# Kernel tuning notes

Measured on AMD Instinct MI355X. Metric: run time of the kernel, lower is better.

Reference implementation:

```python
import jax, jax.numpy as jnp
import numpy as np

N, E = 50000, 800000
IN, HID, HEADS, OUT, EDIM = 128, 32, 4, 40, 5
HC = HEADS * HID  # 128, conv1 output width


def setup_inputs() -> dict:
    key = jax.random.key(0)
    ks = jax.random.split(key, 24)
    p = lambda i, shape: (jax.random.normal(ks[i], shape, jnp.float32) * 0.1)
    return {
        "x": jax.random.normal(ks[0], (N, IN), jnp.float32),
        "edge_index": jax.random.randint(ks[1], (2, E), 0, N, jnp.int32),
        "edge_attr": jax.random.normal(ks[2], (E, EDIM), jnp.float32),
        # GATConv layer 1 (in -> hidden, heads=4)
        "W1": p(3, (IN, HC)), "att_src1": p(4, (HEADS, HID)), "att_dst1": p(5, (HEADS, HID)),
        "att_edge1": p(6, (HEADS, HID)), "We1": p(7, (EDIM, HC)), "b1": p(8, (HC,)),
        # GATConv layer 2 (hidden*heads -> out, heads=1)
        "W2": p(9, (HC, OUT)), "att_src2": p(10, (1, OUT)), "att_dst2": p(11, (1, OUT)),
        "att_edge2": p(12, (1, OUT)), "We2": p(13, (EDIM, OUT)), "b2": p(14, (OUT,)),
        # BatchNorm (eval mode: running stats)
        "g1": jnp.ones((HC,), jnp.float32), "be1": p(15, (HC,)),
        "rm1": p(16, (HC,)), "rv1": jnp.ones((HC,), jnp.float32),
        "g2": jnp.ones((OUT,), jnp.float32), "be2": p(17, (OUT,)),
        "rm2": p(18, (OUT,)), "rv2": jnp.ones((OUT,), jnp.float32),
    }


def gat_conv(x, src, dst, eattr, W, a_src, a_dst, a_edge, We, b, H, C):
    n = x.shape[0]
    xs = (x @ W).reshape(n, H, C)                       # shared lin for src/dst (PyG)
    alpha_s = jnp.einsum('nhc,hc->nh', xs, a_src)       # [N,H]
    alpha_d = jnp.einsum('nhc,hc->nh', xs, a_dst)       # [N,H]
    e = (eattr @ We).reshape(-1, H, C)                  # [E',H,C]
    alpha_e = jnp.einsum('ehc,hc->eh', e, a_edge)       # [E',H]
    alpha = jax.nn.leaky_relu(alpha_s[src] + alpha_d[dst] + alpha_e, 0.2)
    # segment softmax over incoming edges of each dst node
    amax = jax.ops.segment_max(alpha, dst, num_segments=n)
    ex = jnp.exp(alpha - amax[dst])
    denom = jax.ops.segment_sum(ex, dst, num_segments=n)
    coef = ex / (denom[dst] + 1e-16)                    # [E',H]
    out = jax.ops.segment_sum(xs[src] * coef[:, :, None], dst, num_segments=n)
    return out.reshape(n, H * C) + b                    # concat heads + bias


def batch_norm_eval(x, g, be, rm, rv):
    return g * (x - rm) * jax.lax.rsqrt(rv + 1e-5) + be


def reference(x, edge_index, edge_attr, W1, att_src1, att_dst1, att_edge1, We1, b1,
              W2, att_src2, att_dst2, att_edge2, We2, b2,
              g1, be1, rm1, rv1, g2, be2, rm2, rv2):
    src0, dst0 = edge_index[0], edge_index[1]
    # add self loops with fill_value='mean': loop edge_attr = mean of incoming edge_attr
    cnt = jax.ops.segment_sum(jnp.ones((E,), x.dtype), dst0, num_segments=N)
    loop_attr = jax.ops.segment_sum(edge_attr, dst0, num_segments=N) / jnp.maximum(cnt, 1.0)[:, None]
    loop = jnp.arange(N, dtype=src0.dtype)
    src = jnp.concatenate([src0, loop])
    dst = jnp.concatenate([dst0, loop])
    ea = jnp.concatenate([edge_attr, loop_attr], axis=0)
    # layer 1 (dropout = identity in eval)
    h = gat_conv(x, src, dst, ea, W1, att_src1, att_dst1, att_edge1, We1, b1, HEADS, HID)
    h = jax.nn.elu(batch_norm_eval(h, g1, be1, rm1, rv1))
    # layer 2 (heads=1)
    h = gat_conv(h, src, dst, ea, W2, att_src2, att_dst2, att_edge2, We2, b2, 1, OUT)
    h = batch_norm_eval(h, g2, be2, rm2, rv2)
    return jax.nn.log_softmax(h, axis=1)
```

## Files before the change

kernel.cpp:

```cpp
#include <hip/hip_runtime.h>
#include <hip/hip_bf16.h>

#define NN 50000
#define NE 800000
#define SCAN_NB ((NN + 255) / 256)

typedef float f32x4_t __attribute__((ext_vector_type(4)));
typedef float f32x2_t __attribute__((ext_vector_type(2)));
typedef short s16x8_t __attribute__((ext_vector_type(8)));

__device__ __forceinline__ unsigned f2bf2(float a, float b) {
    unsigned ua = __float_as_uint(a);
    ua = (ua + 0x7fffu + ((ua >> 16) & 1u)) >> 16;
    unsigned ub = __float_as_uint(b);
    ub = (ub + 0x7fffu + ((ub >> 16) & 1u)) >> 16;
    return ua | (ub << 16);
}
__device__ __forceinline__ float bf_lo(unsigned u) { return __uint_as_float(u << 16); }
__device__ __forceinline__ float bf_hi(unsigned u) { return __uint_as_float(u & 0xffff0000u); }
__device__ __forceinline__ f32x2_t bfpair(unsigned u) {
    return (f32x2_t){__uint_as_float(u << 16), __uint_as_float(u & 0xffff0000u)};
}

__global__ __launch_bounds__(256) void prep_kernel(
    const float* __restrict__ We1, const float* __restrict__ ae1w,
    const float* __restrict__ We2, const float* __restrict__ ae2w,
    const float* __restrict__ W1, const float* __restrict__ W2,
    float* __restrict__ wf1, float* __restrict__ wf2,
    unsigned* __restrict__ w1t, unsigned* __restrict__ w2t,
    int* __restrict__ cnt) {
    int t = threadIdx.x;
    int g = blockIdx.x * 256 + t;
    if (g < NN) cnt[g] = 0;
    if (blockIdx.x != 0) return;
    if (t < 20) {
        int j = t >> 2, h = t & 3;
        float s = 0.f;
        for (int c = 0; c < 32; ++c) s += We1[j * 128 + h * 32 + c] * ae1w[h * 32 + c];
        wf1[j * 4 + h] = s;
    }
    if (t >= 32 && t < 37) {
        int j = t - 32;
        float s = 0.f;
        for (int c = 0; c < 40; ++c) s += We2[j * 40 + c] * ae2w[c];
        wf2[j] = s;
    }
    for (int i = t; i < 128 * 64; i += 256) {
        int c = i >> 6, kp = i & 63;
        w1t[i] = f2bf2(W1[(size_t)(2 * kp) * 128 + c], W1[(size_t)(2 * kp + 1) * 128 + c]);
    }
    for (int i = t; i < 48 * 64; i += 256) {
        int c = i >> 6, kp = i & 63;
        w2t[i] = (c < 40) ? f2bf2(W2[(size_t)(2 * kp) * 40 + c], W2[(size_t)(2 * kp + 1) * 40 + c]) : 0u;
    }
}

__global__ __launch_bounds__(256) void count_kernel(const int* __restrict__ dst0,
                                                    int* __restrict__ cnt,
                                                    int* __restrict__ rank) {
    int e = blockIdx.x * 256 + threadIdx.x;
    if (e >= NE) return;
    rank[e] = atomicAdd(&cnt[dst0[e]], 1);
}

__global__ __launch_bounds__(256) void scan1_kernel(const int* __restrict__ cnt,
                                                    int* __restrict__ off,
                                                    int* __restrict__ bsum) {
    __shared__ int tmp[256];
    int t = threadIdx.x;
    int g = blockIdx.x * 256 + t;
    int v = (g < NN) ? cnt[g] : 0;
    tmp[t] = v;
    __syncthreads();
#pragma unroll
    for (int d = 1; d < 256; d <<= 1) {
        int u = (t >= d) ? tmp[t - d] : 0;
        __syncthreads();
        tmp[t] += u;
        __syncthreads();
    }
    if (g < NN) off[g] = tmp[t] - v;
    if (t == 255) bsum[blockIdx.x] = tmp[255];
}

__global__ __launch_bounds__(256) void scan2_kernel(int* __restrict__ bsum) {
    __shared__ int tmp[256];
    int t = threadIdx.x;
    int v = (t < SCAN_NB) ? bsum[t] : 0;
    tmp[t] = v;
    __syncthreads();
#pragma unroll
    for (int d = 1; d < 256; d <<= 1) {
        int u = (t >= d) ? tmp[t - d] : 0;
        __syncthreads();
        tmp[t] += u;
        __syncthreads();
    }
    if (t < SCAN_NB) bsum[t] = tmp[t] - v;
}

__global__ __launch_bounds__(256) void scan3_kernel(int* __restrict__ off,
                                                    const int* __restrict__ bsum,
                                                    const int* __restrict__ cnt) {
    int g = blockIdx.x * 256 + threadIdx.x;
    if (g < NN) {
        int o = off[g] + bsum[blockIdx.x];
        off[g] = o;
        if (g == NN - 1) off[NN] = o + cnt[g];
    }
}

__global__ __launch_bounds__(256) void fill_fold_kernel(
    const int* __restrict__ src0, const int* __restrict__ dst0,
    const float* __restrict__ eattr, const float* __restrict__ wf1,
    const float* __restrict__ wf2, const int* __restrict__ off,
    const int* __restrict__ rank, uint4* __restrict__ epk) {
    int base = blockIdx.x * 1024 + threadIdx.x;
#pragma unroll
    for (int k = 0; k < 4; ++k) {
        int e = base + k * 256;
        if (e >= NE) continue;
        float a[5];
#pragma unroll
        for (int j = 0; j < 5; ++j) a[j] = eattr[(size_t)e * 5 + j];
        float o[4];
#pragma unroll
        for (int h = 0; h < 4; ++h) {
            float s = 0.f;
#pragma unroll
            for (int j = 0; j < 5; ++j) s += a[j] * wf1[j * 4 + h];
            o[h] = s;
        }
        float s2 = 0.f;
#pragma unroll
        for (int j = 0; j < 5; ++j) s2 += a[j] * wf2[j];
        int pos = off[dst0[e]] + rank[e];
        epk[pos] = make_uint4((unsigned)src0[e], f2bf2(o[0], o[1]), f2bf2(o[2], o[3]),
                              __float_as_uint(s2));
    }
}

__global__ __launch_bounds__(256) void gemm1_mfma(
    const float* __restrict__ A, const unsigned* __restrict__ w1t,
    unsigned* __restrict__ out) {
    __shared__ unsigned sA[64 * 68];
    __shared__ unsigned sB[128 * 68];
    int t = threadIdx.x;
    int row0 = blockIdx.x * 64;
    for (int i = t; i < 64 * 32; i += 256) {
        int r = i >> 5, q = i & 31;
        int gr = row0 + r;
        float4 v = (gr < NN) ? *(const float4*)&A[(size_t)gr * 128 + q * 4]
                             : make_float4(0.f, 0.f, 0.f, 0.f);
        sA[r * 68 + q * 2]     = f2bf2(v.x, v.y);
        sA[r * 68 + q * 2 + 1] = f2bf2(v.z, v.w);
    }
    for (int i = t; i < 128 * 16; i += 256) {
        int c = i >> 4, q = i & 15;
        *(uint4*)&sB[c * 68 + q * 4] = *(const uint4*)&w1t[c * 64 + q * 4];
    }
    __syncthreads();
    int wv = t >> 6, lane = t & 63;
    int lr = lane & 15, kgrp = lane >> 4;
    f32x4_t acc[8];
#pragma unroll
    for (int i = 0; i < 8; ++i) acc[i] = (f32x4_t){0.f, 0.f, 0.f, 0.f};
    int arow = wv * 16 + lr;
#pragma unroll
    for (int kt = 0; kt < 4; ++kt) {
        int kw = kt * 16 + kgrp * 4;
        s16x8_t af = *(const s16x8_t*)&sA[arow * 68 + kw];
#pragma unroll
        for (int tc = 0; tc < 8; ++tc) {
            s16x8_t bf = *(const s16x8_t*)&sB[(tc * 16 + lr) * 68 + kw];
            acc[tc] = __builtin_amdgcn_mfma_f32_16x16x32_bf16(af, bf, acc[tc], 0, 0, 0);
        }
    }
    int orow0 = row0 + wv * 16 + kgrp * 4;
#pragma unroll
    for (int tc = 0; tc < 8; ++tc) {
#pragma unroll
        for (int r = 0; r < 4; ++r) {
            float v = acc[tc][r];
            float other = __shfl_xor(v, 1);
            int gr = orow0 + r;
            if (!(lane & 1) && gr < NN)
                out[(size_t)gr * 64 + tc * 8 + (lr >> 1)] = f2bf2(v, other);
        }
    }
}

__global__ __launch_bounds__(256) void alpha1_kernel(
    const unsigned* __restrict__ xs1u, const float* __restrict__ asw,
    const float* __restrict__ adw, float* __restrict__ as1, float* __restrict__ ad1) {
    int wid = (blockIdx.x * 256 + threadIdx.x) >> 6;
    if (wid >= NN) return;
    int lane = threadIdx.x & 63;
    int c = lane * 2;
    unsigned u = xs1u[(size_t)wid * 64 + lane];
    float vx = bf_lo(u), vy = bf_hi(u);
    float pa = vx * asw[c] + vy * asw[c + 1];
    float pd = vx * adw[c] + vy * adw[c + 1];
#pragma unroll
    for (int d = 8; d >= 1; d >>= 1) {
        pa += __shfl_xor(pa, d, 16);
        pd += __shfl_xor(pd, d, 16);
    }
    if ((lane & 15) == 0) {
        as1[wid * 4 + (lane >> 4)] = pa;
        ad1[wid * 4 + (lane >> 4)] = pd;
    }
}

__global__ __launch_bounds__(256) void gat1_kernel(
    const uint4* __restrict__ epk, const int* __restrict__ off,
    const unsigned* __restrict__ xs1u,
    const float4* __restrict__ as1, const float4* __restrict__ ad1,
    const float* __restrict__ b1, const float* __restrict__ g1, const float* __restrict__ be1,
    const float* __restrict__ rm1, const float* __restrict__ rv1, unsigned* __restrict__ h1u) {
    __shared__ int   lds_s[4][4][16];
    __shared__ float lds_w[4][4][16][4];
    int wave = threadIdx.x >> 6;
    int lane = threadIdx.x & 63;
    int g = lane >> 4;
    int lr = lane & 15;
    int qh = lr >> 2;
    int n = blockIdx.x * 16 + wave * 4 + g;
    int e0 = off[n];
    int deg = off[n + 1] - e0;
    float4 adn = ad1[n];
    float4 asn = as1[n];
    f32x2_t acc2[4];
#pragma unroll
    for (int k = 0; k < 4; ++k) acc2[k] = (f32x2_t){0.f, 0.f};
    float ds0 = 0.f, ds1 = 0.f, ds2 = 0.f, ds3 = 0.f;
    float s0 = 0.f, s1 = 0.f, s2 = 0.f, s3 = 0.f;
    int mc = (deg + 15) >> 4;
    mc = max(mc, __shfl_xor(mc, 16));
    mc = max(mc, __shfl_xor(mc, 32));

    for (int ch = 0; ch < mc; ++ch) {
        int i = ch * 16 + lr;
        int s = 0;
        float w0 = 0.f, w1 = 0.f, w2 = 0.f, w3 = 0.f;
        if (i < deg) {
            uint4 ep = epk[e0 + i];
            s = (int)ep.x;
            float ax = bf_lo(ep.y), ay = bf_hi(ep.y);
            float az = bf_lo(ep.z), aw = bf_hi(ep.z);
            float4 av = as1[s];
            float a0 = av.x + adn.x + ax;
            float a1 = av.y + adn.y + ay;
            float a2 = av.z + adn.z + az;
            float a3 = av.w + adn.w + aw;
            a0 = a0 >= 0.f ? a0 : 0.2f * a0;
            a1 = a1 >= 0.f ? a1 : 0.2f * a1;
            a2 = a2 >= 0.f ? a2 : 0.2f * a2;
            a3 = a3 >= 0.f ? a3 : 0.2f * a3;
            w0 = __expf(a0); w1 = __expf(a1); w2 = __expf(a2); w3 = __expf(a3);
            ds0 += w0; ds1 += w1; ds2 += w2; ds3 += w3;
            s0 += ax; s1 += ay; s2 += az; s3 += aw;
        }
        lds_s[wave][g][lr] = s;
        *(float4*)&lds_w[wave][g][lr][0] = make_float4(w0, w1, w2, w3);
        __builtin_amdgcn_wave_barrier();
        int cn = deg - ch * 16;
        cn = cn > 16 ? 16 : (cn < 0 ? 0 : cn);
        int cnr = (cn + 3) & ~3;
        for (int j = 0; j < cnr; j += 4) {
            int sj0 = lds_s[wave][g][j];
            int sj1 = lds_s[wave][g][j + 1];
            int sj2 = lds_s[wave][g][j + 2];
            int sj3 = lds_s[wave][g][j + 3];
            float ww0 = lds_w[wave][g][j][qh];
            float ww1 = lds_w[wave][g][j + 1][qh];
            float ww2 = lds_w[wave][g][j + 2][qh];
            float ww3 = lds_w[wave][g][j + 3][qh];
            uint4 u0 = *(const uint4*)&xs1u[(size_t)sj0 * 64 + lr * 4];
            uint4 u1 = *(const uint4*)&xs1u[(size_t)sj1 * 64 + lr * 4];
            uint4 u2 = *(const uint4*)&xs1u[(size_t)sj2 * 64 + lr * 4];
            uint4 u3 = *(const uint4*)&xs1u[(size_t)sj3 * 64 + lr * 4];
            f32x2_t W0 = {ww0, ww0}, W1v = {ww1, ww1}, W2v = {ww2, ww2}, W3v = {ww3, ww3};
            acc2[0] += W0 * bfpair(u0.x); acc2[1] += W0 * bfpair(u0.y);
            acc2[2] += W0 * bfpair(u0.z); acc2[3] += W0 * bfpair(u0.w);
            acc2[0] += W1v * bfpair(u1.x); acc2[1] += W1v * bfpair(u1.y);
            acc2[2] += W1v * bfpair(u1.z); acc2[3] += W1v * bfpair(u1.w);
            acc2[0] += W2v * bfpair(u2.x); acc2[1] += W2v * bfpair(u2.y);
            acc2[2] += W2v * bfpair(u2.z); acc2[3] += W2v * bfpair(u2.w);
            acc2[0] += W3v * bfpair(u3.x); acc2[1] += W3v * bfpair(u3.y);
            acc2[2] += W3v * bfpair(u3.z); acc2[3] += W3v * bfpair(u3.w);
        }
        __builtin_amdgcn_wave_barrier();
    }
#pragma unroll
    for (int d = 8; d >= 1; d >>= 1) {
        ds0 += __shfl_xor(ds0, d, 16); ds1 += __shfl_xor(ds1, d, 16);
        ds2 += __shfl_xor(ds2, d, 16); ds3 += __shfl_xor(ds3, d, 16);
        s0 += __shfl_xor(s0, d, 16);   s1 += __shfl_xor(s1, d, 16);
        s2 += __shfl_xor(s2, d, 16);   s3 += __shfl_xor(s3, d, 16);
    }
    float invd = 1.f / fmaxf((float)deg, 1.f);
    float aL0 = asn.x + adn.x + s0 * invd;
    float aL1 = asn.y + adn.y + s1 * invd;
    float aL2 = asn.z + adn.z + s2 * invd;
    float aL3 = asn.w + adn.w + s3 * invd;
    aL0 = aL0 >= 0.f ? aL0 : 0.2f * aL0;
    aL1 = aL1 >= 0.f ? aL1 : 0.2f * aL1;
    aL2 = aL2 >= 0.f ? aL2 : 0.2f * aL2;
    aL3 = aL3 >= 0.f ? aL3 : 0.2f * aL3;
    float ws0 = __expf(aL0), ws1 = __expf(aL1), ws2 = __expf(aL2), ws3 = __expf(aL3);
    float wself = qh == 0 ? ws0 : (qh == 1 ? ws1 : (qh == 2 ? ws2 : ws3));
    float dh = qh == 0 ? ds0 + ws0 : (qh == 1 ? ds1 + ws1 : (qh == 2 ? ds2 + ws2 : ds3 + ws3));
    uint4 us = *(const uint4*)&xs1u[(size_t)n * 64 + lr * 4];
    f32x2_t Ws = {wself, wself};
    acc2[0] += Ws * bfpair(us.x); acc2[1] += Ws * bfpair(us.y);
    acc2[2] += Ws * bfpair(us.z); acc2[3] += Ws * bfpair(us.w);
    float inv = 1.f / (dh + 1e-16f);
    int c = lr * 8;
    uint4 ou;
    unsigned* op = (unsigned*)&ou;
#pragma unroll
    for (int k2 = 0; k2 < 4; ++k2) {
        int c0 = c + 2 * k2, c1 = c + 2 * k2 + 1;
        float o0 = acc2[k2][0] * inv + b1[c0];
        float o1 = acc2[k2][1] * inv + b1[c1];
        float sc0 = g1[c0] * rsqrtf(rv1[c0] + 1e-5f);
        float sc1 = g1[c1] * rsqrtf(rv1[c1] + 1e-5f);
        o0 = (o0 - rm1[c0]) * sc0 + be1[c0];
        o1 = (o1 - rm1[c1]) * sc1 + be1[c1];
        o0 = o0 > 0.f ? o0 : __expf(o0) - 1.f;
        o1 = o1 > 0.f ? o1 : __expf(o1) - 1.f;
        op[k2] = f2bf2(o0, o1);
    }
    *(uint4*)&h1u[(size_t)n * 64 + lr * 4] = ou;
}

__global__ __launch_bounds__(256) void gemm2_mfma(
    const unsigned* __restrict__ A, const unsigned* __restrict__ w2t,
    unsigned* __restrict__ out) {
    __shared__ unsigned sA[64 * 68];
    __shared__ unsigned sB[48 * 68];
    int t = threadIdx.x;
    int row0 = blockIdx.x * 64;
    for (int i = t; i < 64 * 16; i += 256) {
        int r = i >> 4, q = i & 15;
        int gr = row0 + r;
        uint4 v = (gr < NN) ? *(const uint4*)&A[(size_t)gr * 64 + q * 4]
                            : make_uint4(0u, 0u, 0u, 0u);
        *(uint4*)&sA[r * 68 + q * 4] = v;
    }
    for (int i = t; i < 48 * 16; i += 256) {
        int c = i >> 4, q = i & 15;
        *(uint4*)&sB[c * 68 + q * 4] = *(const uint4*)&w2t[c * 64 + q * 4];
    }
    __syncthreads();
    int wv = t >> 6, lane = t & 63;
    int lr = lane & 15, kgrp = lane >> 4;
    f32x4_t acc[3];
#pragma unroll
    for (int i = 0; i < 3; ++i) acc[i] = (f32x4_t){0.f, 0.f, 0.f, 0.f};
    int arow = wv * 16 + lr;
#pragma unroll
    for (int kt = 0; kt < 4; ++kt) {
        int kw = kt * 16 + kgrp * 4;
        s16x8_t af = *(const s16x8_t*)&sA[arow * 68 + kw];
#pragma unroll
        for (int tc = 0; tc < 3; ++tc) {
            s16x8_t bf = *(const s16x8_t*)&sB[(tc * 16 + lr) * 68 + kw];
            acc[tc] = __builtin_amdgcn_mfma_f32_16x16x32_bf16(af, bf, acc[tc], 0, 0, 0);
        }
    }
    int orow0 = row0 + wv * 16 + kgrp * 4;
#pragma unroll
    for (int tc = 0; tc < 3; ++tc) {
#pragma unroll
        for (int r = 0; r < 4; ++r) {
            float v = acc[tc][r];
            float other = __shfl_xor(v, 1);
            int gr = orow0 + r;
            if (!(lane & 1) && gr < NN && (tc < 2 || lr < 8))
                out[(size_t)gr * 32 + tc * 8 + (lr >> 1)] = f2bf2(v, other);
        }
    }
}

__global__ __launch_bounds__(256) void alpha2_kernel(
    const unsigned* __restrict__ xs2u, const float* __restrict__ asw,
    const float* __restrict__ adw, float* __restrict__ as2, float* __restrict__ ad2) {
    int wid = (blockIdx.x * 256 + threadIdx.x) >> 6;
    if (wid >= NN) return;
    int lane = threadIdx.x & 63;
    float pa = 0.f, pd = 0.f;
    if (lane < 20) {
        unsigned u = xs2u[(size_t)wid * 32 + lane];
        float vx = bf_lo(u), vy = bf_hi(u);
        int c = lane * 2;
        pa = vx * asw[c] + vy * asw[c + 1];
        pd = vx * adw[c] + vy * adw[c + 1];
    }
#pragma unroll
    for (int d = 16; d >= 1; d >>= 1) {
        pa += __shfl_xor(pa, d, 32);
        pd += __shfl_xor(pd, d, 32);
    }
    if (lane == 0) { as2[wid] = pa; ad2[wid] = pd; }
}

__global__ __launch_bounds__(256) void gat2_kernel(
    const uint4* __restrict__ epk, const int* __restrict__ off,
    const unsigned* __restrict__ xs2u,
    const float* __restrict__ as2, const float* __restrict__ ad2,
    const float* __restrict__ b2, const float* __restrict__ g2, const float* __restrict__ be2,
    const float* __restrict__ rm2, const float* __restrict__ rv2, float* __restrict__ outp) {
    __shared__ int   lds_s[4][72];
    __shared__ float lds_w[4][72];
    int wid = (blockIdx.x * 256 + threadIdx.x) >> 6;
    if (wid >= NN) return;
    int lane = threadIdx.x & 63;
    int warp = threadIdx.x >> 6;
    int n = wid;
    int e0 = off[n], e1 = off[n + 1];
    int deg = e1 - e0;
    int grp3 = lane / 20;
    int col = lane - grp3 * 20;
    bool act = grp3 < 3;
    int grpo = act ? grp3 : 0;
    if (lane < 8) {
        lds_s[warp][64 + lane] = 0;
        lds_w[warp][64 + lane] = 0.f;
    }
    float adn = ad2[n];
    float asn = as2[n];
    f32x2_t acc2 = {0.f, 0.f};
    float dsum = 0.f, aesum = 0.f;

    for (int base = 0; base < deg; base += 64) {
        int i = base + lane;
        int cn = min(64, deg - base);
        int s = 0;
        float w = 0.f;
        if (i < deg) {
            uint4 ep = epk[e0 + i];
            s = (int)ep.x;
            float ae = __uint_as_float(ep.w);
            float a = as2[s] + adn + ae;
            a = a >= 0.f ? a : 0.2f * a;
            w = __expf(a);
            dsum += w;
            aesum += ae;
        }
        lds_s[warp][lane] = s;
        lds_w[warp][lane] = w;
        __builtin_amdgcn_wave_barrier();
        int cnr = ((cn + 11) / 12) * 12;
        for (int j = 0; j < cnr; j += 12) {
            int jj0 = j + grpo, jj1 = jj0 + 3, jj2 = jj0 + 6, jj3 = jj0 + 9;
            int sj0 = lds_s[warp][jj0];
            int sj1 = lds_s[warp][jj1];
            int sj2 = lds_s[warp][jj2];
            int sj3 = lds_s[warp][jj3];
            float w0 = act ? lds_w[warp][jj0] : 0.f;
            float w1 = act ? lds_w[warp][jj1] : 0.f;
            float w2 = act ? lds_w[warp][jj2] : 0.f;
            float w3 = act ? lds_w[warp][jj3] : 0.f;
            unsigned u0 = xs2u[(size_t)sj0 * 32 + col];
            unsigned u1 = xs2u[(size_t)sj1 * 32 + col];
            unsigned u2 = xs2u[(size_t)sj2 * 32 + col];
            unsigned u3 = xs2u[(size_t)sj3 * 32 + col];
            acc2 += (f32x2_t){w0, w0} * bfpair(u0);
            acc2 += (f32x2_t){w1, w1} * bfpair(u1);
            acc2 += (f32x2_t){w2, w2} * bfpair(u2);
            acc2 += (f32x2_t){w3, w3} * bfpair(u3);
        }
        __builtin_amdgcn_wave_barrier();
    }
    {
        float p0 = __shfl(acc2[0], (lane + 20) & 63);
        float p1 = __shfl(acc2[1], (lane + 20) & 63);
        float q0 = __shfl(acc2[0], (lane + 40) & 63);
        float q1 = __shfl(acc2[1], (lane + 40) & 63);
        acc2[0] += p0 + q0;
        acc2[1] += p1 + q1;
    }
#pragma unroll
    for (int d = 32; d >= 1; d >>= 1) {
        dsum += __shfl_xor(dsum, d);
        aesum += __shfl_xor(aesum, d);
    }
    float invd = 1.f / fmaxf((float)deg, 1.f);
    float aL = asn + adn + aesum * invd;
    aL = aL >= 0.f ? aL : 0.2f * aL;
    float wself = __expf(aL);
    float denom = dsum + wself;

    float v0 = 0.f, v1 = 0.f;
    if (lane < 20) {
        unsigned u = xs2u[(size_t)n * 32 + lane];
        acc2[0] += wself * bf_lo(u);
        acc2[1] += wself * bf_hi(u);
        int c = lane * 2;
        float inv = 1.f / (denom + 1e-16f);
        v0 = acc2[0] * inv + b2[c];
        v1 = acc2[1] * inv + b2[c + 1];
        float sc0 = g2[c] * rsqrtf(rv2[c] + 1e-5f);
        float sc1 = g2[c + 1] * rsqrtf(rv2[c + 1] + 1e-5f);
        v0 = (v0 - rm2[c]) * sc0 + be2[c];
        v1 = (v1 - rm2[c + 1]) * sc1 + be2[c + 1];
    }
    float mx = (lane < 20) ? fmaxf(v0, v1) : -3.0e38f;
#pragma unroll
    for (int d = 32; d >= 1; d >>= 1) mx = fmaxf(mx, __shfl_xor(mx, d));
    float ex = (lane < 20) ? __expf(v0 - mx) + __expf(v1 - mx) : 0.f;
#pragma unroll
    for (int d = 32; d >= 1; d >>= 1) ex += __shfl_xor(ex, d);
    if (lane < 20) {
        float ls = __logf(ex);
        *(float2*)&outp[(size_t)n * 40 + lane * 2] = make_float2(v0 - mx - ls, v1 - mx - ls);
    }
}

extern "C" void kernel_launch(void* const* d_in, const int* in_sizes, int n_in,
                              void* d_out, int out_size, void* d_ws, size_t ws_size,
                              hipStream_t stream) {
    const float* x     = (const float*)d_in[0];
    const int*   ei    = (const int*)d_in[1];
    const float* eattr = (const float*)d_in[2];
    const float* W1    = (const float*)d_in[3];
    const float* as1w  = (const float*)d_in[4];
    const float* ad1w  = (const float*)d_in[5];
    const float* ae1w  = (const float*)d_in[6];
    const float* We1   = (const float*)d_in[7];
    const float* b1    = (const float*)d_in[8];
    const float* W2    = (const float*)d_in[9];
    const float* as2w  = (const float*)d_in[10];
    const float* ad2w  = (const float*)d_in[11];
    const float* ae2w  = (const float*)d_in[12];
    const float* We2   = (const float*)d_in[13];
    const float* b2    = (const float*)d_in[14];
    const float* g1    = (const float*)d_in[15];
    const float* be1   = (const float*)d_in[16];
    const float* rm1   = (const float*)d_in[17];
    const float* rv1   = (const float*)d_in[18];
    const float* g2    = (const float*)d_in[19];
    const float* be2   = (const float*)d_in[20];
    const float* rm2   = (const float*)d_in[21];
    const float* rv2   = (const float*)d_in[22];

    const int* src0 = ei;
    const int* dst0 = ei + NE;

    char* p = (char*)d_ws;
    auto take = [&](size_t nbytes) {
        void* r = (void*)p;
        p += (nbytes + 255) & ~(size_t)255;
        return r;
    };
    float*    wf1    = (float*)take(80);
    float*    wf2    = (float*)take(20);
    unsigned* w1t    = (unsigned*)take((size_t)128 * 64 * 4);
    unsigned* w2t    = (unsigned*)take((size_t)48 * 64 * 4);
    int*      cnt    = (int*)take((size_t)NN * 4);
    int*      off    = (int*)take((size_t)(NN + 1) * 4);
    int*      bsum   = (int*)take((size_t)SCAN_NB * 4);
    int*      rank   = (int*)take((size_t)NE * 4);
    uint4*    epk    = (uint4*)take((size_t)NE * 16);
    float*    as1    = (float*)take((size_t)NN * 16);
    float*    ad1    = (float*)take((size_t)NN * 16);
    float*    as2    = (float*)take((size_t)NN * 4);
    float*    ad2    = (float*)take((size_t)NN * 4);
    unsigned* xs1u   = (unsigned*)take((size_t)NN * 256);
    unsigned* h1u    = (unsigned*)take((size_t)NN * 256);
    unsigned* xs2u   = (unsigned*)take((size_t)NN * 128);

    prep_kernel<<<SCAN_NB, 256, 0, stream>>>(We1, ae1w, We2, ae2w, W1, W2, wf1, wf2,
                                             w1t, w2t, cnt);
    count_kernel<<<(NE + 255) / 256, 256, 0, stream>>>(dst0, cnt, rank);
    scan1_kernel<<<SCAN_NB, 256, 0, stream>>>(cnt, off, bsum);
    scan2_kernel<<<1, 256, 0, stream>>>(bsum);
    scan3_kernel<<<SCAN_NB, 256, 0, stream>>>(off, bsum, cnt);
    fill_fold_kernel<<<(NE + 1023) / 1024, 256, 0, stream>>>(src0, dst0, eattr, wf1, wf2,
                                                             off, rank, epk);
    gemm1_mfma<<<(NN + 63) / 64, 256, 0, stream>>>(x, w1t, xs1u);
    alpha1_kernel<<<(NN + 3) / 4, 256, 0, stream>>>(xs1u, as1w, ad1w, as1, ad1);
    gat1_kernel<<<NN / 16, 256, 0, stream>>>(epk, off, xs1u, (const float4*)as1,
                                             (const float4*)ad1, b1, g1, be1, rm1, rv1, h1u);
    gemm2_mfma<<<(NN + 63) / 64, 256, 0, stream>>>(h1u, w2t, xs2u);
    alpha2_kernel<<<(NN + 3) / 4, 256, 0, stream>>>(xs2u, as2w, ad2w, as2, ad2);
    gat2_kernel<<<(NN + 3) / 4, 256, 0, stream>>>(epk, off, xs2u, as2, ad2,
                                                  b2, g2, be2, rm2, rv2, (float*)d_out);
}
```

Measured before the change: 180.1 us.

## Fuse independent launches and merge gat1, gemm2, alpha2 into one kernel

Result: no change. 182.4 us (+1.3%).

```diff
diff --git a/kernel.cpp b/kernel.cpp
--- a/kernel.cpp
+++ b/kernel.cpp
@@ -4,6 +4,9 @@
 #define NN 50000
 #define NE 800000
 #define SCAN_NB ((NN + 255) / 256)
+#define CNT_NB ((NE + 255) / 256)
+#define G1_NB ((NN + 63) / 64)
+#define A1_NB ((NN + 3) / 4)
 
 typedef float f32x4_t __attribute__((ext_vector_type(4)));
 typedef float f32x2_t __attribute__((ext_vector_type(2)));
@@ -55,32 +58,101 @@
     }
 }
 
-__global__ __launch_bounds__(256) void count_kernel(const int* __restrict__ dst0,
-                                                    int* __restrict__ cnt,
-                                                    int* __restrict__ rank) {
-    int e = blockIdx.x * 256 + threadIdx.x;
-    if (e >= NE) return;
-    rank[e] = atomicAdd(&cnt[dst0[e]], 1);
-}
-
-__global__ __launch_bounds__(256) void scan1_kernel(const int* __restrict__ cnt,
-                                                    int* __restrict__ off,
-                                                    int* __restrict__ bsum) {
-    __shared__ int tmp[256];
+__global__ __launch_bounds__(256) void count_gemm1(
+    const int* __restrict__ dst0, int* __restrict__ cnt, int* __restrict__ rank,
+    const float* __restrict__ A, const unsigned* __restrict__ w1t,
+    unsigned* __restrict__ out) {
+    if (blockIdx.x < CNT_NB) {
+        int e = blockIdx.x * 256 + threadIdx.x;
+        if (e < NE) rank[e] = atomicAdd(&cnt[dst0[e]], 1);
+        return;
+    }
+    __shared__ unsigned sA[64 * 68];
+    __shared__ unsigned sB[128 * 68];
     int t = threadIdx.x;
-    int g = blockIdx.x * 256 + t;
-    int v = (g < NN) ? cnt[g] : 0;
-    tmp[t] = v;
+    int row0 = (blockIdx.x - CNT_NB) * 64;
+    for (int i = t; i < 64 * 32; i += 256) {
+        int r = i >> 5, q = i & 31;
+        int gr = row0 + r;
+        float4 v = (gr < NN) ? *(const float4*)&A[(size_t)gr * 128 + q * 4]
+                             : make_float4(0.f, 0.f, 0.f, 0.f);
+        sA[r * 68 + q * 2]     = f2bf2(v.x, v.y);
+        sA[r * 68 + q * 2 + 1] = f2bf2(v.z, v.w);
+    }
+    for (int i = t; i < 128 * 16; i += 256) {
+        int c = i >> 4, q = i & 15;
+        *(uint4*)&sB[c * 68 + q * 4] = *(const uint4*)&w1t[c * 64 + q * 4];
+    }
     __syncthreads();
-#pragma unroll
-    for (int d = 1; d < 256; d <<= 1) {
-        int u = (t >= d) ? tmp[t - d] : 0;
+    int wv = t >> 6, lane = t & 63;
+    int lr = lane & 15, kgrp = lane >> 4;
+    f32x4_t acc[8];
+#pragma unroll
+    for (int i = 0; i < 8; ++i) acc[i] = (f32x4_t){0.f, 0.f, 0.f, 0.f};
+    int arow = wv * 16 + lr;
+#pragma unroll
+    for (int kt = 0; kt < 4; ++kt) {
+        int kw = kt * 16 + kgrp * 4;
+        s16x8_t af = *(const s16x8_t*)&sA[arow * 68 + kw];
+#pragma unroll
+        for (int tc = 0; tc < 8; ++tc) {
+            s16x8_t bf = *(const s16x8_t*)&sB[(tc * 16 + lr) * 68 + kw];
+            acc[tc] = __builtin_amdgcn_mfma_f32_16x16x32_bf16(af, bf, acc[tc], 0, 0, 0);
+        }
+    }
+    int orow0 = row0 + wv * 16 + kgrp * 4;
+#pragma unroll
+    for (int tc = 0; tc < 8; ++tc) {
+#pragma unroll
+        for (int r = 0; r < 4; ++r) {
+            float v = acc[tc][r];
+            float other = __shfl_xor(v, 1);
+            int gr = orow0 + r;
+            if (!(lane & 1) && gr < NN)
+                out[(size_t)gr * 64 + tc * 8 + (lr >> 1)] = f2bf2(v, other);
+        }
+    }
+}
+
+__global__ __launch_bounds__(256) void scan1_alpha1(
+    const int* __restrict__ cnt, int* __restrict__ off, int* __restrict__ bsum,
+    const unsigned* __restrict__ xs1u, const float* __restrict__ asw,
+    const float* __restrict__ adw, float* __restrict__ as1, float* __restrict__ ad1) {
+    if (blockIdx.x < SCAN_NB) {
+        __shared__ int tmp[256];
+        int t = threadIdx.x;
+        int g = blockIdx.x * 256 + t;
+        int v = (g < NN) ? cnt[g] : 0;
+        tmp[t] = v;
         __syncthreads();
-        tmp[t] += u;
-        __syncthreads();
-    }
-    if (g < NN) off[g] = tmp[t] - v;
-    if (t == 255) bsum[blockIdx.x] = tmp[255];
+#pragma unroll
+        for (int d = 1; d < 256; d <<= 1) {
+            int u = (t >= d) ? tmp[t - d] : 0;
+            __syncthreads();
+            tmp[t] += u;
+            __syncthreads();
+        }
+        if (g < NN) off[g] = tmp[t] - v;
+        if (t == 255) bsum[blockIdx.x] = tmp[255];
+        return;
+    }
+    int wid = ((blockIdx.x - SCAN_NB) * 256 + threadIdx.x) >> 6;
+    if (wid >= NN) return;
+    int lane = threadIdx.x & 63;
+    int c = lane * 2;
+    unsigned u = xs1u[(size_t)wid * 64 + lane];
+    float vx = bf_lo(u), vy = bf_hi(u);
+    float pa = vx * asw[c] + vy * asw[c + 1];
+    float pd = vx * adw[c] + vy * adw[c + 1];
+#pragma unroll
+    for (int d = 8; d >= 1; d >>= 1) {
+        pa += __shfl_xor(pa, d, 16);
+        pd += __shfl_xor(pd, d, 16);
+    }
+    if ((lane & 15) == 0) {
+        as1[wid * 4 + (lane >> 4)] = pa;
+        ad1[wid * 4 + (lane >> 4)] = pd;
+    }
 }
 
 __global__ __launch_bounds__(256) void scan2_kernel(int* __restrict__ bsum) {
@@ -140,96 +212,45 @@
     }
 }
 
-__global__ __launch_bounds__(256) void gemm1_mfma(
-    const float* __restrict__ A, const unsigned* __restrict__ w1t,
-    unsigned* __restrict__ out) {
-    __shared__ unsigned sA[64 * 68];
-    __shared__ unsigned sB[128 * 68];
-    int t = threadIdx.x;
-    int row0 = blockIdx.x * 64;
-    for (int i = t; i < 64 * 32; i += 256) {
-        int r = i >> 5, q = i & 31;
-        int gr = row0 + r;
-        float4 v = (gr < NN) ? *(const float4*)&A[(size_t)gr * 128 + q * 4]
-                             : make_float4(0.f, 0.f, 0.f, 0.f);
-        sA[r * 68 + q * 2]     = f2bf2(v.x, v.y);
-        sA[r * 68 + q * 2 + 1] = f2bf2(v.z, v.w);
-    }
-    for (int i = t; i < 128 * 16; i += 256) {
-        int c = i >> 4, q = i & 15;
-        *(uint4*)&sB[c * 68 + q * 4] = *(const uint4*)&w1t[c * 64 + q * 4];
-    }
-    __syncthreads();
-    int wv = t >> 6, lane = t & 63;
-    int lr = lane & 15, kgrp = lane >> 4;
-    f32x4_t acc[8];
-#pragma unroll
-    for (int i = 0; i < 8; ++i) acc[i] = (f32x4_t){0.f, 0.f, 0.f, 0.f};
-    int arow = wv * 16 + lr;
-#pragma unroll
-    for (int kt = 0; kt < 4; ++kt) {
-        int kw = kt * 16 + kgrp * 4;
-        s16x8_t af = *(const s16x8_t*)&sA[arow * 68 + kw];
-#pragma unroll
-        for (int tc = 0; tc < 8; ++tc) {
-            s16x8_t bf = *(const s16x8_t*)&sB[(tc * 16 + lr) * 68 + kw];
-            acc[tc] = __builtin_amdgcn_mfma_f32_16x16x32_bf16(af, bf, acc[tc], 0, 0, 0);
-        }
-    }
-    int orow0 = row0 + wv * 16 + kgrp * 4;
-#pragma unroll
-    for (int tc = 0; tc < 8; ++tc) {
-#pragma unroll
-        for (int r = 0; r < 4; ++r) {
-            float v = acc[tc][r];
-            float other = __shfl_xor(v, 1);
-            int gr = orow0 + r;
-            if (!(lane & 1) && gr < NN)
-                out[(size_t)gr * 64 + tc * 8 + (lr >> 1)] = f2bf2(v, other);
-        }
-    }
-}
-
-__global__ __launch_bounds__(256) void alpha1_kernel(
-    const unsigned* __restrict__ xs1u, const float* __restrict__ asw,
-    const float* __restrict__ adw, float* __restrict__ as1, float* __restrict__ ad1) {
-    int wid = (blockIdx.x * 256 + threadIdx.x) >> 6;
-    if (wid >= NN) return;
-    int lane = threadIdx.x & 63;
-    int c = lane * 2;
-    unsigned u = xs1u[(size_t)wid * 64 + lane];
-    float vx = bf_lo(u), vy = bf_hi(u);
-    float pa = vx * asw[c] + vy * asw[c + 1];
-    float pd = vx * adw[c] + vy * adw[c + 1];
-#pragma unroll
-    for (int d = 8; d >= 1; d >>= 1) {
-        pa += __shfl_xor(pa, d, 16);
-        pd += __shfl_xor(pd, d, 16);
-    }
-    if ((lane & 15) == 0) {
-        as1[wid * 4 + (lane >> 4)] = pa;
-        ad1[wid * 4 + (lane >> 4)] = pd;
-    }
-}
-
-__global__ __launch_bounds__(256) void gat1_kernel(
+__global__ __launch_bounds__(1024) void layer2_fused(
     const uint4* __restrict__ epk, const int* __restrict__ off,
     const unsigned* __restrict__ xs1u,
     const float4* __restrict__ as1, const float4* __restrict__ ad1,
     const float* __restrict__ b1, const float* __restrict__ g1, const float* __restrict__ be1,
-    const float* __restrict__ rm1, const float* __restrict__ rv1, unsigned* __restrict__ h1u) {
-    __shared__ int   lds_s[4][4][16];
-    __shared__ float lds_w[4][4][16][4];
-    int wave = threadIdx.x >> 6;
-    int lane = threadIdx.x & 63;
+    const float* __restrict__ rm1, const float* __restrict__ rv1,
+    const unsigned* __restrict__ w2t, const float* __restrict__ as2w,
+    const float* __restrict__ ad2w, unsigned* __restrict__ xs2u,
+    float* __restrict__ as2, float* __restrict__ ad2) {
+    __shared__ unsigned hA[64 * 68];
+    __shared__ unsigned sB[48 * 68];
+    __shared__ int   lds_s[16][4][16];
+    __shared__ float lds_w[16][4][16][4];
+    __shared__ unsigned hX[64 * 24];
+
+    int tid = threadIdx.x;
+    int wave = tid >> 6;
+    int lane = tid & 63;
     int g = lane >> 4;
     int lr = lane & 15;
     int qh = lr >> 2;
-    int n = blockIdx.x * 16 + wave * 4 + g;
-    int e0 = off[n];
-    int deg = off[n + 1] - e0;
-    float4 adn = ad1[n];
-    float4 asn = as1[n];
+    int row0 = blockIdx.x * 64;
+    int rhat = wave * 4 + g;
+    int n = row0 + rhat;
+    bool valid = n < NN;
+
+    if (tid < 48 * 16) {
+        int c = tid >> 4, q = tid & 15;
+        *(uint4*)&sB[c * 68 + q * 4] = *(const uint4*)&w2t[c * 64 + q * 4];
+    }
+
+    int e0 = 0, deg = 0;
+    float4 adn = make_float4(0.f, 0.f, 0.f, 0.f), asn = adn;
+    if (valid) {
+        e0 = off[n];
+        deg = off[n + 1] - e0;
+        adn = ad1[n];
+        asn = as1[n];
+    }
     f32x2_t acc2[4];
 #pragma unroll
     for (int k = 0; k < 4; ++k) acc2[k] = (f32x2_t){0.f, 0.f};
@@ -299,111 +320,90 @@
         s0 += __shfl_xor(s0, d, 16);   s1 += __shfl_xor(s1, d, 16);
         s2 += __shfl_xor(s2, d, 16);   s3 += __shfl_xor(s3, d, 16);
     }
-    float invd = 1.f / fmaxf((float)deg, 1.f);
-    float aL0 = asn.x + adn.x + s0 * invd;
-    float aL1 = asn.y + adn.y + s1 * invd;
-    float aL2 = asn.z + adn.z + s2 * invd;
-    float aL3 = asn.w + adn.w + s3 * invd;
-    aL0 = aL0 >= 0.f ? aL0 : 0.2f * aL0;
-    aL1 = aL1 >= 0.f ? aL1 : 0.2f * aL1;
-    aL2 = aL2 >= 0.f ? aL2 : 0.2f * aL2;
-    aL3 = aL3 >= 0.f ? aL3 : 0.2f * aL3;
-    float ws0 = __expf(aL0), ws1 = __expf(aL1), ws2 = __expf(aL2), ws3 = __expf(aL3);
-    float wself = qh == 0 ? ws0 : (qh == 1 ? ws1 : (qh == 2 ? ws2 : ws3));
-    float dh = qh == 0 ? ds0 + ws0 : (qh == 1 ? ds1 + ws1 : (qh == 2 ? ds2 + ws2 : ds3 + ws3));
-    uint4 us = *(const uint4*)&xs1u[(size_t)n * 64 + lr * 4];
-    f32x2_t Ws = {wself, wself};
-    acc2[0] += Ws * bfpair(us.x); acc2[1] += Ws * bfpair(us.y);
-    acc2[2] += Ws * bfpair(us.z); acc2[3] += Ws * bfpair(us.w);
-    float inv = 1.f / (dh + 1e-16f);
-    int c = lr * 8;
-    uint4 ou;
-    unsigned* op = (unsigned*)&ou;
-#pragma unroll
-    for (int k2 = 0; k2 < 4; ++k2) {
-        int c0 = c + 2 * k2, c1 = c + 2 * k2 + 1;
-        float o0 = acc2[k2][0] * inv + b1[c0];
-        float o1 = acc2[k2][1] * inv + b1[c1];
-        float sc0 = g1[c0] * rsqrtf(rv1[c0] + 1e-5f);
-        float sc1 = g1[c1] * rsqrtf(rv1[c1] + 1e-5f);
-        o0 = (o0 - rm1[c0]) * sc0 + be1[c0];
-        o1 = (o1 - rm1[c1]) * sc1 + be1[c1];
-        o0 = o0 > 0.f ? o0 : __expf(o0) - 1.f;
-        o1 = o1 > 0.f ? o1 : __expf(o1) - 1.f;
-        op[k2] = f2bf2(o0, o1);
-    }
-    *(uint4*)&h1u[(size_t)n * 64 + lr * 4] = ou;
-}
-
-__global__ __launch_bounds__(256) void gemm2_mfma(
-    const unsigned* __restrict__ A, const unsigned* __restrict__ w2t,
-    unsigned* __restrict__ out) {
-    __shared__ unsigned sA[64 * 68];
-    __shared__ unsigned sB[48 * 68];
-    int t = threadIdx.x;
-    int row0 = blockIdx.x * 64;
-    for (int i = t; i < 64 * 16; i += 256) {
-        int r = i >> 4, q = i & 15;
-        int gr = row0 + r;
-        uint4 v = (gr < NN) ? *(const uint4*)&A[(size_t)gr * 64 + q * 4]
-                            : make_uint4(0u, 0u, 0u, 0u);
-        *(uint4*)&sA[r * 68 + q * 4] = v;
-    }
-    for (int i = t; i < 48 * 16; i += 256) {
-        int c = i >> 4, q = i & 15;
-        *(uint4*)&sB[c * 68 + q * 4] = *(const uint4*)&w2t[c * 64 + q * 4];
-    }
+    uint4 ou = make_uint4(0u, 0u, 0u, 0u);
+    if (valid) {
+        float invd = 1.f / fmaxf((float)deg, 1.f);
+        float aL0 = asn.x + adn.x + s0 * invd;
+        float aL1 = asn.y + adn.y + s1 * invd;
+        float aL2 = asn.z + adn.z + s2 * invd;
+        float aL3 = asn.w + adn.w + s3 * invd;
+        aL0 = aL0 >= 0.f ? aL0 : 0.2f * aL0;
+        aL1 = aL1 >= 0.f ? aL1 : 0.2f * aL1;
+        aL2 = aL2 >= 0.f ? aL2 : 0.2f * aL2;
+        aL3 = aL3 >= 0.f ? aL3 : 0.2f * aL3;
+        float ws0 = __expf(aL0), ws1 = __expf(aL1), ws2 = __expf(aL2), ws3 = __expf(aL3);
+        float wself = qh == 0 ? ws0 : (qh == 1 ? ws1 : (qh == 2 ? ws2 : ws3));
+        float dh = qh == 0 ? ds0 + ws0 : (qh == 1 ? ds1 + ws1 : (qh == 2 ? ds2 + ws2 : ds3 + ws3));
+        uint4 us = *(const uint4*)&xs1u[(size_t)n * 64 + lr * 4];
+        f32x2_t Ws = {wself, wself};
+        acc2[0] += Ws * bfpair(us.x); acc2[1] += Ws * bfpair(us.y);
+        acc2[2] += Ws * bfpair(us.z); acc2[3] += Ws * bfpair(us.w);
+        float inv = 1.f / (dh + 1e-16f);
+        int c = lr * 8;
+        unsigned* op = (unsigned*)&ou;
+#pragma unroll
+        for (int k2 = 0; k2 < 4; ++k2) {
+            int c0 = c + 2 * k2, c1 = c + 2 * k2 + 1;
+            float o0 = acc2[k2][0] * inv + b1[c0];
+            float o1 = acc2[k2][1] * inv + b1[c1];
+            float sc0 = g1[c0] * rsqrtf(rv1[c0] + 1e-5f);
+            float sc1 = g1[c1] * rsqrtf(rv1[c1] + 1e-5f);
+            o0 = (o0 - rm1[c0]) * sc0 + be1[c0];
+            o1 = (o1 - rm1[c1]) * sc1 + be1[c1];
+            o0 = o0 > 0.f ? o0 : __expf(o0) - 1.f;
+            o1 = o1 > 0.f ? o1 : __expf(o1) - 1.f;
+            op[k2] = f2bf2(o0, o1);
+        }
+    }
+    *(uint4*)&hA[rhat * 68 + lr * 4] = ou;
     __syncthreads();
-    int wv = t >> 6, lane = t & 63;
-    int lr = lane & 15, kgrp = lane >> 4;
-    f32x4_t acc[3];
-#pragma unroll
-    for (int i = 0; i < 3; ++i) acc[i] = (f32x4_t){0.f, 0.f, 0.f, 0.f};
-    int arow = wv * 16 + lr;
-#pragma unroll
-    for (int kt = 0; kt < 4; ++kt) {
-        int kw = kt * 16 + kgrp * 4;
-        s16x8_t af = *(const s16x8_t*)&sA[arow * 68 + kw];
-#pragma unroll
-        for (int tc = 0; tc < 3; ++tc) {
+
+    if (wave < 12) {
+        int rowgrp = wave & 3, tc = wave >> 2;
+        int kgrp = lane >> 4;
+        int arow = rowgrp * 16 + lr;
+        f32x4_t acc = (f32x4_t){0.f, 0.f, 0.f, 0.f};
+#pragma unroll
+        for (int kt = 0; kt < 4; ++kt) {
+            int kw = kt * 16 + kgrp * 4;
+            s16x8_t af = *(const s16x8_t*)&hA[arow * 68 + kw];
             s16x8_t bf = *(const s16x8_t*)&sB[(tc * 16 + lr) * 68 + kw];
-            acc[tc] = __builtin_amdgcn_mfma_f32_16x16x32_bf16(af, bf, acc[tc], 0, 0, 0);
-        }
-    }
-    int orow0 = row0 + wv * 16 + kgrp * 4;
-#pragma unroll
-    for (int tc = 0; tc < 3; ++tc) {
+            acc = __builtin_amdgcn_mfma_f32_16x16x32_bf16(af, bf, acc, 0, 0, 0);
+        }
+        int orow = rowgrp * 16 + kgrp * 4;
 #pragma unroll
         for (int r = 0; r < 4; ++r) {
-            float v = acc[tc][r];
+            float v = acc[r];
             float other = __shfl_xor(v, 1);
-            int gr = orow0 + r;
-            if (!(lane & 1) && gr < NN && (tc < 2 || lr < 8))
-                out[(size_t)gr * 32 + tc * 8 + (lr >> 1)] = f2bf2(v, other);
-        }
-    }
-}
-
-__global__ __launch_bounds__(256) void alpha2_kernel(
-    const unsigned* __restrict__ xs2u, const float* __restrict__ asw,
-    const float* __restrict__ adw, float* __restrict__ as2, float* __restrict__ ad2) {
-    int wid = (blockIdx.x * 256 + threadIdx.x) >> 6;
-    if (wid >= NN) return;
-    int lane = threadIdx.x & 63;
-    float pa = 0.f, pd = 0.f;
-    if (lane < 20) {
-        unsigned u = xs2u[(size_t)wid * 32 + lane];
-        float vx = bf_lo(u), vy = bf_hi(u);
-        int c = lane * 2;
-        pa = vx * asw[c] + vy * asw[c + 1];
-        pd = vx * adw[c] + vy * adw[c + 1];
-    }
-#pragma unroll
-    for (int d = 16; d >= 1; d >>= 1) {
-        pa += __shfl_xor(pa, d, 32);
-        pd += __shfl_xor(pd, d, 32);
-    }
-    if (lane == 0) { as2[wid] = pa; ad2[wid] = pd; }
+            int gr = row0 + orow + r;
+            if (!(lane & 1) && gr < NN && (tc < 2 || lr < 8)) {
+                unsigned u = f2bf2(v, other);
+                xs2u[(size_t)gr * 32 + tc * 8 + (lr >> 1)] = u;
+                hX[(orow + r) * 24 + tc * 8 + (lr >> 1)] = u;
+            }
+        }
+    }
+    __syncthreads();
+
+#pragma unroll
+    for (int k = 0; k < 4; ++k) {
+        int rr = wave * 4 + k;
+        int gr = row0 + rr;
+        float pa = 0.f, pd = 0.f;
+        if (lane < 20) {
+            unsigned u = hX[rr * 24 + lane];
+            float vx = bf_lo(u), vy = bf_hi(u);
+            int c = lane * 2;
+            pa = vx * as2w[c] + vy * as2w[c + 1];
+            pd = vx * ad2w[c] + vy * ad2w[c + 1];
+        }
+#pragma unroll
+        for (int d = 16; d >= 1; d >>= 1) {
+            pa += __shfl_xor(pa, d, 32);
+            pd += __shfl_xor(pd, d, 32);
+        }
+        if (lane == 0 && gr < NN) { as2[gr] = pa; ad2[gr] = pd; }
+    }
 }
 
 __global__ __launch_bounds__(256) void gat2_kernel(
@@ -569,23 +569,20 @@
     float*    as2    = (float*)take((size_t)NN * 4);
     float*    ad2    = (float*)take((size_t)NN * 4);
     unsigned* xs1u   = (unsigned*)take((size_t)NN * 256);
-    unsigned* h1u    = (unsigned*)take((size_t)NN * 256);
     unsigned* xs2u   = (unsigned*)take((size_t)NN * 128);
 
     prep_kernel<<<SCAN_NB, 256, 0, stream>>>(We1, ae1w, We2, ae2w, W1, W2, wf1, wf2,
                                              w1t, w2t, cnt);
-    count_kernel<<<(NE + 255) / 256, 256, 0, stream>>>(dst0, cnt, rank);
-    scan1_kernel<<<SCAN_NB, 256, 0, stream>>>(cnt, off, bsum);
+    count_gemm1<<<CNT_NB + G1_NB, 256, 0, stream>>>(dst0, cnt, rank, x, w1t, xs1u);
+    scan1_alpha1<<<SCAN_NB + A1_NB, 256, 0, stream>>>(cnt, off, bsum, xs1u, as1w, ad1w,
+                                                      as1, ad1);
     scan2_kernel<<<1, 256, 0, stream>>>(bsum);
     scan3_kernel<<<SCAN_NB, 256, 0, stream>>>(off, bsum, cnt);
     fill_fold_kernel<<<(NE + 1023) / 1024, 256, 0, stream>>>(src0, dst0, eattr, wf1, wf2,
                                                              off, rank, epk);
-    gemm1_mfma<<<(NN + 63) / 64, 256, 0, stream>>>(x, w1t, xs1u);
-    alpha1_kernel<<<(NN + 3) / 4, 256, 0, stream>>>(xs1u, as1w, ad1w, as1, ad1);
-    gat1_kernel<<<NN / 16, 256, 0, stream>>>(epk, off, xs1u, (const float4*)as1,
-                                             (const float4*)ad1, b1, g1, be1, rm1, rv1, h1u);
-    gemm2_mfma<<<(NN + 63) / 64, 256, 0, stream>>>(h1u, w2t, xs2u);
-    alpha2_kernel<<<(NN + 3) / 4, 256, 0, stream>>>(xs2u, as2w, ad2w, as2, ad2);
+    layer2_fused<<<G1_NB, 1024, 0, stream>>>(epk, off, xs1u, (const float4*)as1,
+                                             (const float4*)ad1, b1, g1, be1, rm1, rv1,
+                                             w2t, as2w, ad2w, xs2u, as2, ad2);
     gat2_kernel<<<(NN + 3) / 4, 256, 0, stream>>>(epk, off, xs2u, as2, ad2,
                                                   b2, g2, be2, rm2, rv2, (float*)d_out);
 }
```

## Merge independent CSR build and GEMM1 stages into fewer horizontally fused launches

Applied to the files above, without the earlier changes.

After: 172.7 us. 1.04x faster.

```diff
diff --git a/kernel.cpp b/kernel.cpp
--- a/kernel.cpp
+++ b/kernel.cpp
@@ -4,6 +4,9 @@
 #define NN 50000
 #define NE 800000
 #define SCAN_NB ((NN + 255) / 256)
+#define CNT_NB ((NE + 255) / 256)
+#define G1_NB ((NN + 63) / 64)
+#define A1_NB ((NN + 3) / 4)
 
 typedef float f32x4_t __attribute__((ext_vector_type(4)));
 typedef float f32x2_t __attribute__((ext_vector_type(2)));
@@ -55,98 +58,19 @@
     }
 }
 
-__global__ __launch_bounds__(256) void count_kernel(const int* __restrict__ dst0,
-                                                    int* __restrict__ cnt,
-                                                    int* __restrict__ rank) {
-    int e = blockIdx.x * 256 + threadIdx.x;
-    if (e >= NE) return;
-    rank[e] = atomicAdd(&cnt[dst0[e]], 1);
-}
-
-__global__ __launch_bounds__(256) void scan1_kernel(const int* __restrict__ cnt,
-                                                    int* __restrict__ off,
-                                                    int* __restrict__ bsum) {
-    __shared__ int tmp[256];
-    int t = threadIdx.x;
-    int g = blockIdx.x * 256 + t;
-    int v = (g < NN) ? cnt[g] : 0;
-    tmp[t] = v;
-    __syncthreads();
-#pragma unroll
-    for (int d = 1; d < 256; d <<= 1) {
-        int u = (t >= d) ? tmp[t - d] : 0;
-        __syncthreads();
-        tmp[t] += u;
-        __syncthreads();
-    }
-    if (g < NN) off[g] = tmp[t] - v;
-    if (t == 255) bsum[blockIdx.x] = tmp[255];
-}
-
-__global__ __launch_bounds__(256) void scan2_kernel(int* __restrict__ bsum) {
-    __shared__ int tmp[256];
-    int t = threadIdx.x;
-    int v = (t < SCAN_NB) ? bsum[t] : 0;
-    tmp[t] = v;
-    __syncthreads();
-#pragma unroll
-    for (int d = 1; d < 256; d <<= 1) {
-        int u = (t >= d) ? tmp[t - d] : 0;
-        __syncthreads();
-        tmp[t] += u;
-        __syncthreads();
-    }
-    if (t < SCAN_NB) bsum[t] = tmp[t] - v;
-}
-
-__global__ __launch_bounds__(256) void scan3_kernel(int* __restrict__ off,
-                                                    const int* __restrict__ bsum,
-                                                    const int* __restrict__ cnt) {
-    int g = blockIdx.x * 256 + threadIdx.x;
-    if (g < NN) {
-        int o = off[g] + bsum[blockIdx.x];
-        off[g] = o;
-        if (g == NN - 1) off[NN] = o + cnt[g];
-    }
-}
-
-__global__ __launch_bounds__(256) void fill_fold_kernel(
-    const int* __restrict__ src0, const int* __restrict__ dst0,
-    const float* __restrict__ eattr, const float* __restrict__ wf1,
-    const float* __restrict__ wf2, const int* __restrict__ off,
-    const int* __restrict__ rank, uint4* __restrict__ epk) {
-    int base = blockIdx.x * 1024 + threadIdx.x;
-#pragma unroll
-    for (int k = 0; k < 4; ++k) {
-        int e = base + k * 256;
-        if (e >= NE) continue;
-        float a[5];
-#pragma unroll
-        for (int j = 0; j < 5; ++j) a[j] = eattr[(size_t)e * 5 + j];
-        float o[4];
-#pragma unroll
-        for (int h = 0; h < 4; ++h) {
-            float s = 0.f;
-#pragma unroll
-            for (int j = 0; j < 5; ++j) s += a[j] * wf1[j * 4 + h];
-            o[h] = s;
-        }
-        float s2 = 0.f;
-#pragma unroll
-        for (int j = 0; j < 5; ++j) s2 += a[j] * wf2[j];
-        int pos = off[dst0[e]] + rank[e];
-        epk[pos] = make_uint4((unsigned)src0[e], f2bf2(o[0], o[1]), f2bf2(o[2], o[3]),
-                              __float_as_uint(s2));
-    }
-}
-
-__global__ __launch_bounds__(256) void gemm1_mfma(
+__global__ __launch_bounds__(256) void count_gemm1(
+    const int* __restrict__ dst0, int* __restrict__ cnt, int* __restrict__ rank,
     const float* __restrict__ A, const unsigned* __restrict__ w1t,
     unsigned* __restrict__ out) {
+    if (blockIdx.x < CNT_NB) {
+        int e = blockIdx.x * 256 + threadIdx.x;
+        if (e < NE) rank[e] = atomicAdd(&cnt[dst0[e]], 1);
+        return;
+    }
     __shared__ unsigned sA[64 * 68];
     __shared__ unsigned sB[128 * 68];
     int t = threadIdx.x;
-    int row0 = blockIdx.x * 64;
+    int row0 = (blockIdx.x - CNT_NB) * 64;
     for (int i = t; i < 64 * 32; i += 256) {
         int r = i >> 5, q = i & 31;
         int gr = row0 + r;
@@ -190,10 +114,29 @@
     }
 }
 
-__global__ __launch_bounds__(256) void alpha1_kernel(
+__global__ __launch_bounds__(256) void scan1_alpha1(
+    const int* __restrict__ cnt, int* __restrict__ off, int* __restrict__ bsum,
     const unsigned* __restrict__ xs1u, const float* __restrict__ asw,
     const float* __restrict__ adw, float* __restrict__ as1, float* __restrict__ ad1) {
-    int wid = (blockIdx.x * 256 + threadIdx.x) >> 6;
+    if (blockIdx.x < SCAN_NB) {
+        __shared__ int tmp[256];
+        int t = threadIdx.x;
+        int g = blockIdx.x * 256 + t;
+        int v = (g < NN) ? cnt[g] : 0;
+        tmp[t] = v;
+        __syncthreads();
+#pragma unroll
+        for (int d = 1; d < 256; d <<= 1) {
+            int u = (t >= d) ? tmp[t - d] : 0;
+            __syncthreads();
+            tmp[t] += u;
+            __syncthreads();
+        }
+        if (g < NN) off[g] = tmp[t] - v;
+        if (t == 255) bsum[blockIdx.x] = tmp[255];
+        return;
+    }
+    int wid = ((blockIdx.x - SCAN_NB) * 256 + threadIdx.x) >> 6;
     if (wid >= NN) return;
     int lane = threadIdx.x & 63;
     int c = lane * 2;
@@ -209,6 +152,60 @@
     if ((lane & 15) == 0) {
         as1[wid * 4 + (lane >> 4)] = pa;
         ad1[wid * 4 + (lane >> 4)] = pd;
+    }
+}
+
+__global__ __launch_bounds__(256) void scan3_kernel(int* __restrict__ off,
+                                                    const int* __restrict__ bsum,
+                                                    const int* __restrict__ cnt) {
+    __shared__ int tmp[256];
+    int t = threadIdx.x;
+    int v = (t < SCAN_NB) ? bsum[t] : 0;
+    tmp[t] = v;
+    __syncthreads();
+#pragma unroll
+    for (int d = 1; d < 256; d <<= 1) {
+        int u = (t >= d) ? tmp[t - d] : 0;
+        __syncthreads();
+        tmp[t] += u;
+        __syncthreads();
+    }
+    int pre = (blockIdx.x == 0) ? 0 : tmp[blockIdx.x - 1];
+    int g = blockIdx.x * 256 + t;
+    if (g < NN) {
+        int o = off[g] + pre;
+        off[g] = o;
+        if (g == NN - 1) off[NN] = o + cnt[g];
+    }
+}
+
+__global__ __launch_bounds__(256) void fill_fold_kernel(
+    const int* __restrict__ src0, const int* __restrict__ dst0,
+    const float* __restrict__ eattr, const float* __restrict__ wf1,
+    const float* __restrict__ wf2, const int* __restrict__ off,
+    const int* __restrict__ rank, uint4* __restrict__ epk) {
+    int base = blockIdx.x * 1024 + threadIdx.x;
+#pragma unroll
+    for (int k = 0; k < 4; ++k) {
+        int e = base + k * 256;
+        if (e >= NE) continue;
+        float a[5];
+#pragma unroll
+        for (int j = 0; j < 5; ++j) a[j] = eattr[(size_t)e * 5 + j];
+        float o[4];
+#pragma unroll
+        for (int h = 0; h < 4; ++h) {
+            float s = 0.f;
+#pragma unroll
+            for (int j = 0; j < 5; ++j) s += a[j] * wf1[j * 4 + h];
+            o[h] = s;
+        }
+        float s2 = 0.f;
+#pragma unroll
+        for (int j = 0; j < 5; ++j) s2 += a[j] * wf2[j];
+        int pos = off[dst0[e]] + rank[e];
+        epk[pos] = make_uint4((unsigned)src0[e], f2bf2(o[0], o[1]), f2bf2(o[2], o[3]),
+                              __float_as_uint(s2));
     }
 }
 
@@ -574,14 +571,12 @@
 
     prep_kernel<<<SCAN_NB, 256, 0, stream>>>(We1, ae1w, We2, ae2w, W1, W2, wf1, wf2,
                                              w1t, w2t, cnt);
-    count_kernel<<<(NE + 255) / 256, 256, 0, stream>>>(dst0, cnt, rank);
-    scan1_kernel<<<SCAN_NB, 256, 0, stream>>>(cnt, off, bsum);
-    scan2_kernel<<<1, 256, 0, stream>>>(bsum);
+    count_gemm1<<<CNT_NB + G1_NB, 256, 0, stream>>>(dst0, cnt, rank, x, w1t, xs1u);
+    scan1_alpha1<<<SCAN_NB + A1_NB, 256, 0, stream>>>(cnt, off, bsum, xs1u, as1w, ad1w,
+                                                      as1, ad1);
     scan3_kernel<<<SCAN_NB, 256, 0, stream>>>(off, bsum, cnt);
     fill_fold_kernel<<<(NE + 1023) / 1024, 256, 0, stream>>>(src0, dst0, eattr, wf1, wf2,
                                                              off, rank, epk);
-    gemm1_mfma<<<(NN + 63) / 64, 256, 0, stream>>>(x, w1t, xs1u);
-    alpha1_kernel<<<(NN + 3) / 4, 256, 0, stream>>>(xs1u, as1w, ad1w, as1, ad1);
     gat1_kernel<<<NN / 16, 256, 0, stream>>>(epk, off, xs1u, (const float4*)as1,
                                              (const float4*)ad1, b1, g1, be1, rm1, rv1, h1u);
     gemm2_mfma<<<(NN + 63) / 64, 256, 0, stream>>>(h1u, w2t, xs2u);
```
